# Kernel tuning notes

Hardware: AMD Instinct MI355X
Metric: run time of the kernel (lower is better)

The kernel has to match this reference:

```python
import jax, jax.numpy as jnp
import numpy as np

B, C, H, W = 4, 256, 64, 64
DQ = C // 8

def setup_inputs() -> dict:
    key = jax.random.key(0)
    ks = jax.random.split(key, 7)
    x = jax.random.normal(ks[0], (B, C, H, W), dtype=jnp.float32)
    # 1x1 convs == per-pixel linear layers: weight [out, in], bias [out]
    Wq = jax.random.normal(ks[1], (DQ, C), dtype=jnp.float32) * (1.0 / np.sqrt(C))
    bq = jax.random.normal(ks[2], (DQ,), dtype=jnp.float32) * 0.01
    Wk = jax.random.normal(ks[3], (DQ, C), dtype=jnp.float32) * (1.0 / np.sqrt(C))
    bk = jax.random.normal(ks[4], (DQ,), dtype=jnp.float32) * 0.01
    Wv = jax.random.normal(ks[5], (C, C), dtype=jnp.float32) * (1.0 / np.sqrt(C))
    bv = jax.random.normal(ks[6], (C,), dtype=jnp.float32) * 0.01
    return {"x": x, "Wq": Wq, "bq": bq, "Wk": Wk, "bk": bk, "Wv": Wv, "bv": bv}

def reference(x, Wq, bq, Wk, bk, Wv, bv):
    b, c, h, w = x.shape
    n = h * w
    xf = x.reshape(b, c, n)                                  # [b,c,n]
    Q = jnp.einsum('dc,bcn->bnd', Wq, xf) + bq               # [b,n,dq]
    K = jnp.einsum('dc,bcn->bdn', Wk, xf) + bk[None, :, None]  # [b,dq,n]
    A = jax.nn.softmax(jnp.einsum('bnd,bdm->bnm', Q, K), axis=-1)  # [b,n,n]
    V = jnp.einsum('oc,bcn->bon', Wv, xf) + bv[None, :, None]      # [b,c,n]
    # torch: bmm(V, A^T) -> out[b,c,i] = sum_j V[b,c,j] * A[b,i,j]
    out = jnp.einsum('bcj,bij->bci', V, A)
    return x + out.reshape(b, c, h, w)
```

## Files before the change

kernel.cpp:

```cpp
#include <hip/hip_runtime.h>
#include <math.h>

#define BB 4
#define CC 256
#define NN 4096
#define DQ 32
#define LOG2E 1.44269504f

typedef _Float16 half8 __attribute__((ext_vector_type(8)));
typedef _Float16 half4 __attribute__((ext_vector_type(4)));
typedef float float4v __attribute__((ext_vector_type(4)));

__global__ __launch_bounds__(64) void prep_kernel(
    const float* __restrict__ Wq, const float* __restrict__ bq,
    const float* __restrict__ Wk, const float* __restrict__ bk,
    const float* __restrict__ Wv, const float* __restrict__ bv,
    _Float16* __restrict__ Wh, float* __restrict__ bh)
{
    int o = blockIdx.x, t = threadIdx.x;
    const float* src; float scale = 1.0f, bias;
    if (o < DQ)            { src = Wq + o * CC;        scale = LOG2E; bias = bq[o] * LOG2E; }
    else if (o < 2 * DQ)   { src = Wk + (o - DQ) * CC;                bias = bk[o - DQ]; }
    else                   { src = Wv + (o - 2 * DQ) * CC;            bias = bv[o - 2 * DQ]; }
    float4 v = *(const float4*)(src + t * 4);
    half4 h = { (_Float16)(v.x * scale), (_Float16)(v.y * scale),
                (_Float16)(v.z * scale), (_Float16)(v.w * scale) };
    *(half4*)(Wh + o * CC + t * 4) = h;
    if (t == 0) bh[o] = bias;
}

__global__ __launch_bounds__(256) void proj_kernel(
    const float* __restrict__ x, const _Float16* __restrict__ Wh,
    const float* __restrict__ bh,
    _Float16* __restrict__ Qt, _Float16* __restrict__ Kt,
    _Float16* __restrict__ Vh)
{
    __shared__ _Float16 xl[32 * 256];
    __shared__ _Float16 os_qk[32 * 72];
    __shared__ _Float16 os_v[256 * 40];

    const int tid = threadIdx.x;
    const int lane = tid & 63, w = tid >> 6;
    const int i16 = lane & 15, q = lane >> 4;
    const int n0 = blockIdx.x * 32, b = blockIdx.y;

    const float* xb = x + (size_t)b * CC * NN + n0;
    #pragma unroll
    for (int u = 0; u < 8; ++u) {
        int idx = u * 256 + tid;
        int c = idx >> 3, n4 = idx & 7;
        float4 v = *(const float4*)(xb + (size_t)c * NN + n4 * 4);
        int chunk = c >> 3, cl = c & 7;
        float vv[4] = {v.x, v.y, v.z, v.w};
        #pragma unroll
        for (int e = 0; e < 4; ++e) {
            int n = n4 * 4 + e;
            xl[n * 256 + ((chunk ^ n) * 8) + cl] = (_Float16)vv[e];
        }
    }

    float4v acc[5][2];
    const int obase = 80 * w;
    #pragma unroll
    for (int ot = 0; ot < 5; ++ot) {
        float4 b4 = *(const float4*)(bh + obase + 16 * ot + 4 * q);
        #pragma unroll
        for (int nt = 0; nt < 2; ++nt)
            acc[ot][nt] = (float4v){b4.x, b4.y, b4.z, b4.w};
    }
    __syncthreads();

    #pragma unroll
    for (int k = 0; k < 8; ++k) {
        half8 af[5], bf[2];
        #pragma unroll
        for (int ot = 0; ot < 5; ++ot)
            af[ot] = *(const half8*)(Wh + (size_t)(obase + 16 * ot + i16) * CC + k * 32 + 8 * q);
        #pragma unroll
        for (int nt = 0; nt < 2; ++nt) {
            int n = 16 * nt + i16;
            bf[nt] = *(const half8*)&xl[n * 256 + (((4 * k + q) ^ n) * 8)];
        }
        #pragma unroll
        for (int ot = 0; ot < 5; ++ot)
            #pragma unroll
            for (int nt = 0; nt < 2; ++nt)
                acc[ot][nt] = __builtin_amdgcn_mfma_f32_16x16x32_f16(af[ot], bf[nt], acc[ot][nt], 0, 0, 0);
    }

    #pragma unroll
    for (int ot = 0; ot < 5; ++ot) {
        int og = obase + 16 * ot;
        #pragma unroll
        for (int nt = 0; nt < 2; ++nt) {
            int n = 16 * nt + i16;
            if (og < 64) {
                half4 hv = { (_Float16)acc[ot][nt][0], (_Float16)acc[ot][nt][1],
                             (_Float16)acc[ot][nt][2], (_Float16)acc[ot][nt][3] };
                *(half4*)&os_qk[n * 72 + og + 4 * q] = hv;
            } else {
                int cb = og - 64 + 4 * q;
                #pragma unroll
                for (int r = 0; r < 4; ++r)
                    os_v[(cb + r) * 40 + n] = (_Float16)acc[ot][nt][r];
            }
        }
    }
    __syncthreads();

    _Float16* Qtb = Qt + (size_t)b * NN * DQ;
    _Float16* Ktb = Kt + (size_t)b * NN * DQ;
    {
        int n = tid >> 3, p = tid & 7;
        half8 hv = *(const half8*)&os_qk[n * 72 + 8 * p];
        if (p < 4) *(half8*)(Qtb + (size_t)(n0 + n) * DQ + 8 * p) = hv;
        else       *(half8*)(Ktb + (size_t)(n0 + n) * DQ + 8 * (p - 4)) = hv;
    }
    _Float16* Vb = Vh + (size_t)b * CC * NN;
    #pragma unroll
    for (int u = 0; u < 4; ++u) {
        int c = u * 64 + (tid >> 2), p = tid & 3;
        half8 hv = *(const half8*)&os_v[c * 40 + 8 * p];
        *(half8*)(Vb + (size_t)c * NN + n0 + 8 * p) = hv;
    }
}

__global__ __launch_bounds__(256) void rowstat_kernel(
    const _Float16* __restrict__ Qt, const _Float16* __restrict__ Kt,
    float* __restrict__ M2, float* __restrict__ L)
{
    __shared__ _Float16 k_lds[64 * 32];
    const int tid = threadIdx.x;
    const int lane = tid & 63, w = tid >> 6;
    const int i16 = lane & 15, q = lane >> 4;
    const int q0 = blockIdx.x * 64, js = blockIdx.y, b = blockIdx.z;

    const _Float16* Qtb = Qt + (size_t)b * NN * DQ;
    const _Float16* Ktb = Kt + (size_t)b * NN * DQ;
    half8 qb = *(const half8*)(Qtb + (size_t)(q0 + 16 * w + i16) * DQ + 8 * q);

    const int jb = js * 1024;
    const int jl = tid >> 2, dg = tid & 3;
    half8 kv = *(const half8*)(Ktb + (size_t)(jb + jl) * DQ + 8 * dg);

    float m = -INFINITY, l = 0.f;
    for (int t = 0; t < 16; ++t) {
        __syncthreads();
        *(half8*)&k_lds[jl * 32 + ((dg ^ (jl & 3)) * 8)] = kv;
        __syncthreads();
        if (t < 15)
            kv = *(const half8*)(Ktb + (size_t)(jb + (t + 1) * 64 + jl) * DQ + 8 * dg);
        float4v s[4];
        __builtin_amdgcn_s_setprio(1);
        #pragma unroll
        for (int jt = 0; jt < 4; ++jt) {
            int j = 16 * jt + i16;
            half8 ka = *(const half8*)&k_lds[j * 32 + ((q ^ (j & 3)) * 8)];
            float4v z = {0.f, 0.f, 0.f, 0.f};
            s[jt] = __builtin_amdgcn_mfma_f32_16x16x32_f16(ka, qb, z, 0, 0, 0);
        }
        __builtin_amdgcn_s_setprio(0);
        float tmax = s[0][0];
        #pragma unroll
        for (int jt = 0; jt < 4; ++jt)
            #pragma unroll
            for (int r = 0; r < 4; ++r)
                tmax = fmaxf(tmax, s[jt][r]);
        float mnew = fmaxf(m, tmax);
        float sum = 0.f;
        #pragma unroll
        for (int jt = 0; jt < 4; ++jt)
            #pragma unroll
            for (int r = 0; r < 4; ++r)
                sum += exp2f(s[jt][r] - mnew);
        l = l * exp2f(m - mnew) + sum;
        m = mnew;
    }
    #pragma unroll
    for (int off = 16; off <= 32; off <<= 1) {
        float mo = __shfl_xor(m, off, 64);
        float lo = __shfl_xor(l, off, 64);
        float mn = fmaxf(m, mo);
        l = l * exp2f(m - mn) + lo * exp2f(mo - mn);
        m = mn;
    }
    if (q == 0) {
        int qi = q0 + 16 * w + i16;
        M2[((size_t)b * 4 + js) * NN + qi] = m;
        L[((size_t)b * 4 + js) * NN + qi] = l;
    }
}

__global__ __launch_bounds__(256) void attn_kernel(
    const float* __restrict__ x,
    const _Float16* __restrict__ Qt, const _Float16* __restrict__ Kt,
    const _Float16* __restrict__ Vh,
    const float* __restrict__ M2, const float* __restrict__ L,
    float* __restrict__ out)
{
    __shared__ _Float16 k_lds[64 * 32];
    __shared__ _Float16 v_lds[128 * 64];
    __shared__ _Float16 ps[32 * 72];

    const int tid = threadIdx.x;
    const int w = tid >> 6, lane = tid & 63;
    const int i16 = lane & 15, q = lane >> 4;
    const int i0 = blockIdx.x * 32, cs = blockIdx.y, b = blockIdx.z;
    const int c0 = cs * 128;

    const _Float16* Ktb = Kt + (size_t)b * NN * DQ;
    const _Float16* Vb  = Vh + (size_t)b * CC * NN + (size_t)c0 * NN;

    float m2v[2], linv[2];
    #pragma unroll
    for (int it = 0; it < 2; ++it) {
        int qi = i0 + 16 * it + i16;
        float mm = -INFINITY, ll = 0.f;
        #pragma unroll
        for (int p = 0; p < 4; ++p) {
            float mp = M2[((size_t)b * 4 + p) * NN + qi];
            float lp = L [((size_t)b * 4 + p) * NN + qi];
            float mn = fmaxf(mm, mp);
            ll = ll * exp2f(mm - mn) + lp * exp2f(mp - mn);
            mm = mn;
        }
        m2v[it] = mm;
        linv[it] = 1.0f / ll;
    }

    half8 qb[2];
    {
        const _Float16* Qtb = Qt + (size_t)b * NN * DQ;
        qb[0] = *(const half8*)(Qtb + (size_t)(i0 + i16) * DQ + 8 * q);
        qb[1] = *(const half8*)(Qtb + (size_t)(i0 + 16 + i16) * DQ + 8 * q);
    }

    float4v O[2][2];
    #pragma unroll
    for (int ct = 0; ct < 2; ++ct)
        #pragma unroll
        for (int it = 0; it < 2; ++it)
            O[ct][it] = (float4v){0.f, 0.f, 0.f, 0.f};

    const int jK = tid >> 2, dgK = tid & 3;
    const int cbV = tid >> 3, jgV = tid & 7;

    half8 kv, vv[4];
    kv = *(const half8*)(Ktb + (size_t)jK * DQ + 8 * dgK);
    #pragma unroll
    for (int u = 0; u < 4; ++u)
        vv[u] = *(const half8*)(Vb + (size_t)(u * 32 + cbV) * NN + 8 * jgV);

    for (int j0 = 0; j0 < NN; j0 += 64) {
        __syncthreads();
        *(half8*)&k_lds[jK * 32 + ((dgK ^ (jK & 3)) * 8)] = kv;
        #pragma unroll
        for (int u = 0; u < 4; ++u) {
            int c = u * 32 + cbV;
            *(half8*)&v_lds[c * 64 + ((jgV ^ (c & 7)) * 8)] = vv[u];
        }
        __syncthreads();

        if (j0 + 64 < NN) {
            kv = *(const half8*)(Ktb + (size_t)(j0 + 64 + jK) * DQ + 8 * dgK);
            #pragma unroll
            for (int u = 0; u < 4; ++u)
                vv[u] = *(const half8*)(Vb + (size_t)(u * 32 + cbV) * NN + (j0 + 64) + 8 * jgV);
        }

        {
            int j = 16 * w + i16;
            half8 ka = *(const half8*)&k_lds[j * 32 + ((q ^ (j & 3)) * 8)];
            #pragma unroll
            for (int it = 0; it < 2; ++it) {
                float4v z = {0.f, 0.f, 0.f, 0.f};
                float4v s = __builtin_amdgcn_mfma_f32_16x16x32_f16(ka, qb[it], z, 0, 0, 0);
                half4 hv = { (_Float16)exp2f(s[0] - m2v[it]),
                             (_Float16)exp2f(s[1] - m2v[it]),
                             (_Float16)exp2f(s[2] - m2v[it]),
                             (_Float16)exp2f(s[3] - m2v[it]) };
                *(half4*)&ps[(16 * it + i16) * 72 + 16 * w + 4 * q] = hv;
            }
        }
        __syncthreads();

        half8 pb[2][2];
        #pragma unroll
        for (int ks = 0; ks < 2; ++ks)
            #pragma unroll
            for (int it = 0; it < 2; ++it)
                pb[ks][it] = *(const half8*)&ps[(16 * it + i16) * 72 + 32 * ks + 8 * q];
        __builtin_amdgcn_s_setprio(1);
        #pragma unroll
        for (int ct = 0; ct < 2; ++ct) {
            int c = 32 * w + 16 * ct + i16;
            #pragma unroll
            for (int ks = 0; ks < 2; ++ks) {
                int g = 4 * ks + q;
                half8 va = *(const half8*)&v_lds[c * 64 + ((g ^ (c & 7)) * 8)];
                #pragma unroll
                for (int it = 0; it < 2; ++it)
                    O[ct][it] = __builtin_amdgcn_mfma_f32_16x16x32_f16(va, pb[ks][it], O[ct][it], 0, 0, 0);
            }
        }
        __builtin_amdgcn_s_setprio(0);
    }

    const float* xb = x + (size_t)b * CC * NN;
    float* ob = out + (size_t)b * CC * NN;
    #pragma unroll
    for (int ct = 0; ct < 2; ++ct)
        #pragma unroll
        for (int it = 0; it < 2; ++it)
            #pragma unroll
            for (int r = 0; r < 4; ++r) {
                int c = c0 + 32 * w + 16 * ct + 4 * q + r;
                size_t idx = (size_t)c * NN + i0 + 16 * it + i16;
                ob[idx] = xb[idx] + O[ct][it][r] * linv[it];
            }
}

extern "C" void kernel_launch(void* const* d_in, const int* in_sizes, int n_in,
                              void* d_out, int out_size, void* d_ws, size_t ws_size,
                              hipStream_t stream) {
    const float* x  = (const float*)d_in[0];
    const float* Wq = (const float*)d_in[1];
    const float* bq = (const float*)d_in[2];
    const float* Wk = (const float*)d_in[3];
    const float* bk = (const float*)d_in[4];
    const float* Wv = (const float*)d_in[5];
    const float* bv = (const float*)d_in[6];
    float* out = (float*)d_out;

    char* ws = (char*)d_ws;
    _Float16* Wh = (_Float16*)(ws);
    float*    bh = (float*)(ws + 163840);
    _Float16* Qt = (_Float16*)(ws + 262144);
    _Float16* Kt = (_Float16*)(ws + 1310720);
    _Float16* Vh = (_Float16*)(ws + 2359296);
    float*    M2 = (float*)(ws + 10747904);
    float*    L  = (float*)(ws + 11010048);

    prep_kernel<<<dim3(320), 64, 0, stream>>>(Wq, bq, Wk, bk, Wv, bv, Wh, bh);
    proj_kernel<<<dim3(NN / 32, BB), 256, 0, stream>>>(x, Wh, bh, Qt, Kt, Vh);
    rowstat_kernel<<<dim3(NN / 64, 4, BB), 256, 0, stream>>>(Qt, Kt, M2, L);
    attn_kernel<<<dim3(NN / 32, 2, BB), 256, 0, stream>>>(x, Qt, Kt, Vh, M2, L, out);
}
```

Measured before the change: 202.5 us.

## Fuse softmax row statistics into attention via online softmax with double-buffered LDS

Removes the separate rowstat pass that recomputed Q·K over all keys to get the row max and sum. The attention kernel now keeps a running max and sum per row, combining per-wave partial stats through a small shared buffer each tile, and rescales the accumulators and P fragments. K/V tiles are double-buffered in LDS so the next tile's global loads overlap compute, with a single barrier pair per iteration. This adds per-tile shuffles, exp2 rescales and extra LDS traffic, and uses more LDS per block, which may lower occupancy.

```diff
diff --git a/kernel.cpp b/kernel.cpp
--- a/kernel.cpp
+++ b/kernel.cpp
@@ -10,6 +10,7 @@
 typedef _Float16 half8 __attribute__((ext_vector_type(8)));
 typedef _Float16 half4 __attribute__((ext_vector_type(4)));
 typedef float float4v __attribute__((ext_vector_type(4)));
+typedef float float2v __attribute__((ext_vector_type(2)));
 
 __global__ __launch_bounds__(64) void prep_kernel(
     const float* __restrict__ Wq, const float* __restrict__ bq,
@@ -125,82 +126,16 @@
     }
 }
 
-__global__ __launch_bounds__(256) void rowstat_kernel(
-    const _Float16* __restrict__ Qt, const _Float16* __restrict__ Kt,
-    float* __restrict__ M2, float* __restrict__ L)
-{
-    __shared__ _Float16 k_lds[64 * 32];
-    const int tid = threadIdx.x;
-    const int lane = tid & 63, w = tid >> 6;
-    const int i16 = lane & 15, q = lane >> 4;
-    const int q0 = blockIdx.x * 64, js = blockIdx.y, b = blockIdx.z;
-
-    const _Float16* Qtb = Qt + (size_t)b * NN * DQ;
-    const _Float16* Ktb = Kt + (size_t)b * NN * DQ;
-    half8 qb = *(const half8*)(Qtb + (size_t)(q0 + 16 * w + i16) * DQ + 8 * q);
-
-    const int jb = js * 1024;
-    const int jl = tid >> 2, dg = tid & 3;
-    half8 kv = *(const half8*)(Ktb + (size_t)(jb + jl) * DQ + 8 * dg);
-
-    float m = -INFINITY, l = 0.f;
-    for (int t = 0; t < 16; ++t) {
-        __syncthreads();
-        *(half8*)&k_lds[jl * 32 + ((dg ^ (jl & 3)) * 8)] = kv;
-        __syncthreads();
-        if (t < 15)
-            kv = *(const half8*)(Ktb + (size_t)(jb + (t + 1) * 64 + jl) * DQ + 8 * dg);
-        float4v s[4];
-        __builtin_amdgcn_s_setprio(1);
-        #pragma unroll
-        for (int jt = 0; jt < 4; ++jt) {
-            int j = 16 * jt + i16;
-            half8 ka = *(const half8*)&k_lds[j * 32 + ((q ^ (j & 3)) * 8)];
-            float4v z = {0.f, 0.f, 0.f, 0.f};
-            s[jt] = __builtin_amdgcn_mfma_f32_16x16x32_f16(ka, qb, z, 0, 0, 0);
-        }
-        __builtin_amdgcn_s_setprio(0);
-        float tmax = s[0][0];
-        #pragma unroll
-        for (int jt = 0; jt < 4; ++jt)
-            #pragma unroll
-            for (int r = 0; r < 4; ++r)
-                tmax = fmaxf(tmax, s[jt][r]);
-        float mnew = fmaxf(m, tmax);
-        float sum = 0.f;
-        #pragma unroll
-        for (int jt = 0; jt < 4; ++jt)
-            #pragma unroll
-            for (int r = 0; r < 4; ++r)
-                sum += exp2f(s[jt][r] - mnew);
-        l = l * exp2f(m - mnew) + sum;
-        m = mnew;
-    }
-    #pragma unroll
-    for (int off = 16; off <= 32; off <<= 1) {
-        float mo = __shfl_xor(m, off, 64);
-        float lo = __shfl_xor(l, off, 64);
-        float mn = fmaxf(m, mo);
-        l = l * exp2f(m - mn) + lo * exp2f(mo - mn);
-        m = mn;
-    }
-    if (q == 0) {
-        int qi = q0 + 16 * w + i16;
-        M2[((size_t)b * 4 + js) * NN + qi] = m;
-        L[((size_t)b * 4 + js) * NN + qi] = l;
-    }
-}
-
 __global__ __launch_bounds__(256) void attn_kernel(
     const float* __restrict__ x,
     const _Float16* __restrict__ Qt, const _Float16* __restrict__ Kt,
     const _Float16* __restrict__ Vh,
-    const float* __restrict__ M2, const float* __restrict__ L,
     float* __restrict__ out)
 {
-    __shared__ _Float16 k_lds[64 * 32];
-    __shared__ _Float16 v_lds[128 * 64];
+    __shared__ _Float16 k_lds[2][64 * 32];
+    __shared__ _Float16 v_lds[2][128 * 64];
     __shared__ _Float16 ps[32 * 72];
+    __shared__ float    st[32][10];
 
     const int tid = threadIdx.x;
     const int w = tid >> 6, lane = tid & 63;
@@ -211,23 +146,6 @@
     const _Float16* Ktb = Kt + (size_t)b * NN * DQ;
     const _Float16* Vb  = Vh + (size_t)b * CC * NN + (size_t)c0 * NN;
 
-    float m2v[2], linv[2];
-    #pragma unroll
-    for (int it = 0; it < 2; ++it) {
-        int qi = i0 + 16 * it + i16;
-        float mm = -INFINITY, ll = 0.f;
-        #pragma unroll
-        for (int p = 0; p < 4; ++p) {
-            float mp = M2[((size_t)b * 4 + p) * NN + qi];
-            float lp = L [((size_t)b * 4 + p) * NN + qi];
-            float mn = fmaxf(mm, mp);
-            ll = ll * exp2f(mm - mn) + lp * exp2f(mp - mn);
-            mm = mn;
-        }
-        m2v[it] = mm;
-        linv[it] = 1.0f / ll;
-    }
-
     half8 qb[2];
     {
         const _Float16* Qtb = Qt + (size_t)b * NN * DQ;
@@ -241,46 +159,72 @@
         #pragma unroll
         for (int it = 0; it < 2; ++it)
             O[ct][it] = (float4v){0.f, 0.f, 0.f, 0.f};
+    float m_run[2] = {-INFINITY, -INFINITY};
+    float l_run[2] = {0.f, 0.f};
 
     const int jK = tid >> 2, dgK = tid & 3;
     const int cbV = tid >> 3, jgV = tid & 7;
+    const int kaddr = jK * 32 + ((dgK ^ (jK & 3)) * 8);
+    int vaddr[4];
+    #pragma unroll
+    for (int u = 0; u < 4; ++u) {
+        int c = u * 32 + cbV;
+        vaddr[u] = c * 64 + ((jgV ^ (c & 7)) * 8);
+    }
 
     half8 kv, vv[4];
     kv = *(const half8*)(Ktb + (size_t)jK * DQ + 8 * dgK);
     #pragma unroll
     for (int u = 0; u < 4; ++u)
         vv[u] = *(const half8*)(Vb + (size_t)(u * 32 + cbV) * NN + 8 * jgV);
-
-    for (int j0 = 0; j0 < NN; j0 += 64) {
-        __syncthreads();
-        *(half8*)&k_lds[jK * 32 + ((dgK ^ (jK & 3)) * 8)] = kv;
-        #pragma unroll
-        for (int u = 0; u < 4; ++u) {
-            int c = u * 32 + cbV;
-            *(half8*)&v_lds[c * 64 + ((jgV ^ (c & 7)) * 8)] = vv[u];
-        }
-        __syncthreads();
-
-        if (j0 + 64 < NN) {
-            kv = *(const half8*)(Ktb + (size_t)(j0 + 64 + jK) * DQ + 8 * dgK);
+    *(half8*)&k_lds[0][kaddr] = kv;
+    #pragma unroll
+    for (int u = 0; u < 4; ++u)
+        *(half8*)&v_lds[0][vaddr[u]] = vv[u];
+    kv = *(const half8*)(Ktb + (size_t)(64 + jK) * DQ + 8 * dgK);
+    #pragma unroll
+    for (int u = 0; u < 4; ++u)
+        vv[u] = *(const half8*)(Vb + (size_t)(u * 32 + cbV) * NN + 64 + 8 * jgV);
+    __syncthreads();
+
+    for (int t = 0; t < 64; ++t) {
+        const int cur = t & 1;
+
+        if (t < 63) {
+            *(half8*)&k_lds[cur ^ 1][kaddr] = kv;
             #pragma unroll
             for (int u = 0; u < 4; ++u)
-                vv[u] = *(const half8*)(Vb + (size_t)(u * 32 + cbV) * NN + (j0 + 64) + 8 * jgV);
-        }
-
+                *(half8*)&v_lds[cur ^ 1][vaddr[u]] = vv[u];
+        }
         {
             int j = 16 * w + i16;
-            half8 ka = *(const half8*)&k_lds[j * 32 + ((q ^ (j & 3)) * 8)];
+            half8 ka = *(const half8*)&k_lds[cur][j * 32 + ((q ^ (j & 3)) * 8)];
             #pragma unroll
             for (int it = 0; it < 2; ++it) {
                 float4v z = {0.f, 0.f, 0.f, 0.f};
                 float4v s = __builtin_amdgcn_mfma_f32_16x16x32_f16(ka, qb[it], z, 0, 0, 0);
-                half4 hv = { (_Float16)exp2f(s[0] - m2v[it]),
-                             (_Float16)exp2f(s[1] - m2v[it]),
-                             (_Float16)exp2f(s[2] - m2v[it]),
-                             (_Float16)exp2f(s[3] - m2v[it]) };
+                float mx = fmaxf(fmaxf(s[0], s[1]), fmaxf(s[2], s[3]));
+                mx = fmaxf(mx, __shfl_xor(mx, 16));
+                mx = fmaxf(mx, __shfl_xor(mx, 32));
+                float p0 = exp2f(s[0] - mx), p1 = exp2f(s[1] - mx);
+                float p2 = exp2f(s[2] - mx), p3 = exp2f(s[3] - mx);
+                float sm = (p0 + p1) + (p2 + p3);
+                sm += __shfl_xor(sm, 16);
+                sm += __shfl_xor(sm, 32);
+                half4 hv = { (_Float16)p0, (_Float16)p1, (_Float16)p2, (_Float16)p3 };
                 *(half4*)&ps[(16 * it + i16) * 72 + 16 * w + 4 * q] = hv;
+                if (q == 0) {
+                    st[16 * it + i16][2 * w]     = mx;
+                    st[16 * it + i16][2 * w + 1] = sm;
+                }
             }
+        }
+        if (t < 62) {
+            int jn = (t + 2) * 64;
+            kv = *(const half8*)(Ktb + (size_t)(jn + jK) * DQ + 8 * dgK);
+            #pragma unroll
+            for (int u = 0; u < 4; ++u)
+                vv[u] = *(const half8*)(Vb + (size_t)(u * 32 + cbV) * NN + jn + 8 * jgV);
         }
         __syncthreads();
 
@@ -290,6 +234,31 @@
             #pragma unroll
             for (int it = 0; it < 2; ++it)
                 pb[ks][it] = *(const half8*)&ps[(16 * it + i16) * 72 + 32 * ks + 8 * q];
+
+        #pragma unroll
+        for (int it = 0; it < 2; ++it) {
+            const float* sr = &st[16 * it + i16][0];
+            float2v a0 = *(const float2v*)&sr[0];
+            float2v a1 = *(const float2v*)&sr[2];
+            float2v a2 = *(const float2v*)&sr[4];
+            float2v a3 = *(const float2v*)&sr[6];
+            float mt = fmaxf(fmaxf(a0[0], a1[0]), fmaxf(a2[0], a3[0]));
+            float mn = fmaxf(m_run[it], mt);
+            float al = exp2f(m_run[it] - mn);
+            float lt = a0[1] * exp2f(a0[0] - mn) + a1[1] * exp2f(a1[0] - mn)
+                     + a2[1] * exp2f(a2[0] - mn) + a3[1] * exp2f(a3[0] - mn);
+            l_run[it] = l_run[it] * al + lt;
+            m_run[it] = mn;
+            O[0][it] *= al;
+            O[1][it] *= al;
+            float msA = (q & 2) ? a1[0] : a0[0];
+            float msB = (q & 2) ? a3[0] : a2[0];
+            _Float16 bA = (_Float16)exp2f(msA - mn);
+            _Float16 bB = (_Float16)exp2f(msB - mn);
+            pb[0][it] *= bA;
+            pb[1][it] *= bB;
+        }
+
         __builtin_amdgcn_s_setprio(1);
         #pragma unroll
         for (int ct = 0; ct < 2; ++ct) {
@@ -297,15 +266,17 @@
             #pragma unroll
             for (int ks = 0; ks < 2; ++ks) {
                 int g = 4 * ks + q;
-                half8 va = *(const half8*)&v_lds[c * 64 + ((g ^ (c & 7)) * 8)];
+                half8 va = *(const half8*)&v_lds[cur][c * 64 + ((g ^ (c & 7)) * 8)];
                 #pragma unroll
                 for (int it = 0; it < 2; ++it)
                     O[ct][it] = __builtin_amdgcn_mfma_f32_16x16x32_f16(va, pb[ks][it], O[ct][it], 0, 0, 0);
             }
         }
         __builtin_amdgcn_s_setprio(0);
-    }
-
+        __syncthreads();
+    }
+
+    float linv[2] = { 1.0f / l_run[0], 1.0f / l_run[1] };
     const float* xb = x + (size_t)b * CC * NN;
     float* ob = out + (size_t)b * CC * NN;
     #pragma unroll
@@ -338,11 +309,8 @@
     _Float16* Qt = (_Float16*)(ws + 262144);
     _Float16* Kt = (_Float16*)(ws + 1310720);
     _Float16* Vh = (_Float16*)(ws + 2359296);
-    float*    M2 = (float*)(ws + 10747904);
-    float*    L  = (float*)(ws + 11010048);
 
     prep_kernel<<<dim3(320), 64, 0, stream>>>(Wq, bq, Wk, bk, Wv, bv, Wh, bh);
     proj_kernel<<<dim3(NN / 32, BB), 256, 0, stream>>>(x, Wh, bh, Qt, Kt, Vh);
-    rowstat_kernel<<<dim3(NN / 64, 4, BB), 256, 0, stream>>>(Qt, Kt, M2, L);
-    attn_kernel<<<dim3(NN / 32, 2, BB), 256, 0, stream>>>(x, Qt, Kt, Vh, M2, L, out);
+    attn_kernel<<<dim3(NN / 32, 2, BB), 256, 0, stream>>>(x, Qt, Kt, Vh, out);
 }
```

After: 285.4 us. 40.9% more time.

## Pipeline attention QK/PV stages with multi-buffered LDS and drop softmax max rescaling

Applied to the files above, without the earlier changes.

The attention kernel now processes 64 query rows per block and software-pipelines the loop: K and V tiles are double- and triple-buffered in LDS, and P tiles are double-buffered, so the PV MFMA of the previous tile overlaps the QK/exp of the current one with one barrier per iteration. The rowstat kernel drops LDS and online rescaling, reading K fragments straight from global with register prefetch and summing raw exp2 values. The final max is folded into the normalizer. This removes barriers and exp work, but summing unshifted exp2 risks overflow for large logits and the larger tile uses more LDS and registers, which lowers occupancy.

```diff
diff --git a/kernel.cpp b/kernel.cpp
--- a/kernel.cpp
+++ b/kernel.cpp
@@ -129,61 +129,37 @@
     const _Float16* __restrict__ Qt, const _Float16* __restrict__ Kt,
     float* __restrict__ M2, float* __restrict__ L)
 {
-    __shared__ _Float16 k_lds[64 * 32];
     const int tid = threadIdx.x;
     const int lane = tid & 63, w = tid >> 6;
     const int i16 = lane & 15, q = lane >> 4;
     const int q0 = blockIdx.x * 64, js = blockIdx.y, b = blockIdx.z;
 
     const _Float16* Qtb = Qt + (size_t)b * NN * DQ;
-    const _Float16* Ktb = Kt + (size_t)b * NN * DQ;
+    const _Float16* kb  = Kt + (size_t)b * NN * DQ + (size_t)(js * 1024) * DQ;
     half8 qb = *(const half8*)(Qtb + (size_t)(q0 + 16 * w + i16) * DQ + 8 * q);
 
-    const int jb = js * 1024;
-    const int jl = tid >> 2, dg = tid & 3;
-    half8 kv = *(const half8*)(Ktb + (size_t)(jb + jl) * DQ + 8 * dg);
+    half8 ka[4];
+    #pragma unroll
+    for (int u = 0; u < 4; ++u)
+        ka[u] = *(const half8*)(kb + (size_t)(16 * u + i16) * DQ + 8 * q);
 
     float m = -INFINITY, l = 0.f;
-    for (int t = 0; t < 16; ++t) {
-        __syncthreads();
-        *(half8*)&k_lds[jl * 32 + ((dg ^ (jl & 3)) * 8)] = kv;
-        __syncthreads();
-        if (t < 15)
-            kv = *(const half8*)(Ktb + (size_t)(jb + (t + 1) * 64 + jl) * DQ + 8 * dg);
-        float4v s[4];
-        __builtin_amdgcn_s_setprio(1);
-        #pragma unroll
-        for (int jt = 0; jt < 4; ++jt) {
-            int j = 16 * jt + i16;
-            half8 ka = *(const half8*)&k_lds[j * 32 + ((q ^ (j & 3)) * 8)];
+    for (int t = 0; t < 64; t += 4) {
+        #pragma unroll
+        for (int u = 0; u < 4; ++u) {
             float4v z = {0.f, 0.f, 0.f, 0.f};
-            s[jt] = __builtin_amdgcn_mfma_f32_16x16x32_f16(ka, qb, z, 0, 0, 0);
-        }
-        __builtin_amdgcn_s_setprio(0);
-        float tmax = s[0][0];
-        #pragma unroll
-        for (int jt = 0; jt < 4; ++jt)
-            #pragma unroll
-            for (int r = 0; r < 4; ++r)
-                tmax = fmaxf(tmax, s[jt][r]);
-        float mnew = fmaxf(m, tmax);
-        float sum = 0.f;
-        #pragma unroll
-        for (int jt = 0; jt < 4; ++jt)
-            #pragma unroll
-            for (int r = 0; r < 4; ++r)
-                sum += exp2f(s[jt][r] - mnew);
-        l = l * exp2f(m - mnew) + sum;
-        m = mnew;
-    }
-    #pragma unroll
-    for (int off = 16; off <= 32; off <<= 1) {
-        float mo = __shfl_xor(m, off, 64);
-        float lo = __shfl_xor(l, off, 64);
-        float mn = fmaxf(m, mo);
-        l = l * exp2f(m - mn) + lo * exp2f(mo - mn);
-        m = mn;
-    }
+            float4v s = __builtin_amdgcn_mfma_f32_16x16x32_f16(ka[u], qb, z, 0, 0, 0);
+            int nt = t + 4 + u;
+            if (nt < 64)
+                ka[u] = *(const half8*)(kb + (size_t)(16 * nt + i16) * DQ + 8 * q);
+            m = fmaxf(m, fmaxf(fmaxf(s[0], s[1]), fmaxf(s[2], s[3])));
+            l += (exp2f(s[0]) + exp2f(s[1])) + (exp2f(s[2]) + exp2f(s[3]));
+        }
+    }
+    l += __shfl_xor(l, 16, 64);
+    l += __shfl_xor(l, 32, 64);
+    m = fmaxf(m, __shfl_xor(m, 16, 64));
+    m = fmaxf(m, __shfl_xor(m, 32, 64));
     if (q == 0) {
         int qi = q0 + 16 * w + i16;
         M2[((size_t)b * 4 + js) * NN + qi] = m;
@@ -198,112 +174,127 @@
     const float* __restrict__ M2, const float* __restrict__ L,
     float* __restrict__ out)
 {
-    __shared__ _Float16 k_lds[64 * 32];
-    __shared__ _Float16 v_lds[128 * 64];
-    __shared__ _Float16 ps[32 * 72];
+    __shared__ _Float16 k_lds[2][64 * 32];
+    __shared__ _Float16 v_lds[3][128 * 64];
+    __shared__ _Float16 ps[2][64 * 72];
 
     const int tid = threadIdx.x;
     const int w = tid >> 6, lane = tid & 63;
     const int i16 = lane & 15, q = lane >> 4;
-    const int i0 = blockIdx.x * 32, cs = blockIdx.y, b = blockIdx.z;
+    const int i0 = blockIdx.x * 64, cs = blockIdx.y, b = blockIdx.z;
     const int c0 = cs * 128;
 
     const _Float16* Ktb = Kt + (size_t)b * NN * DQ;
     const _Float16* Vb  = Vh + (size_t)b * CC * NN + (size_t)c0 * NN;
 
-    float m2v[2], linv[2];
-    #pragma unroll
-    for (int it = 0; it < 2; ++it) {
+    float m2v[4], linv[4];
+    #pragma unroll
+    for (int it = 0; it < 4; ++it) {
         int qi = i0 + 16 * it + i16;
         float mm = -INFINITY, ll = 0.f;
         #pragma unroll
         for (int p = 0; p < 4; ++p) {
-            float mp = M2[((size_t)b * 4 + p) * NN + qi];
-            float lp = L [((size_t)b * 4 + p) * NN + qi];
-            float mn = fmaxf(mm, mp);
-            ll = ll * exp2f(mm - mn) + lp * exp2f(mp - mn);
-            mm = mn;
+            mm = fmaxf(mm, M2[((size_t)b * 4 + p) * NN + qi]);
+            ll += L[((size_t)b * 4 + p) * NN + qi];
         }
         m2v[it] = mm;
-        linv[it] = 1.0f / ll;
-    }
-
-    half8 qb[2];
+        linv[it] = exp2f(mm) / ll;
+    }
+
+    half8 qb[4];
     {
         const _Float16* Qtb = Qt + (size_t)b * NN * DQ;
-        qb[0] = *(const half8*)(Qtb + (size_t)(i0 + i16) * DQ + 8 * q);
-        qb[1] = *(const half8*)(Qtb + (size_t)(i0 + 16 + i16) * DQ + 8 * q);
-    }
-
-    float4v O[2][2];
+        #pragma unroll
+        for (int it = 0; it < 4; ++it)
+            qb[it] = *(const half8*)(Qtb + (size_t)(i0 + 16 * it + i16) * DQ + 8 * q);
+    }
+
+    float4v O[2][4];
     #pragma unroll
     for (int ct = 0; ct < 2; ++ct)
         #pragma unroll
-        for (int it = 0; it < 2; ++it)
+        for (int it = 0; it < 4; ++it)
             O[ct][it] = (float4v){0.f, 0.f, 0.f, 0.f};
 
     const int jK = tid >> 2, dgK = tid & 3;
     const int cbV = tid >> 3, jgV = tid & 7;
+    const int kaddr = jK * 32 + ((dgK ^ (jK & 3)) * 8);
+    int vaddr[4];
+    #pragma unroll
+    for (int u = 0; u < 4; ++u) {
+        int c = u * 32 + cbV;
+        vaddr[u] = c * 64 + ((jgV ^ (c & 7)) * 8);
+    }
 
     half8 kv, vv[4];
     kv = *(const half8*)(Ktb + (size_t)jK * DQ + 8 * dgK);
     #pragma unroll
     for (int u = 0; u < 4; ++u)
         vv[u] = *(const half8*)(Vb + (size_t)(u * 32 + cbV) * NN + 8 * jgV);
-
-    for (int j0 = 0; j0 < NN; j0 += 64) {
+    *(half8*)&k_lds[0][kaddr] = kv;
+    #pragma unroll
+    for (int u = 0; u < 4; ++u)
+        *(half8*)&v_lds[0][vaddr[u]] = vv[u];
+    kv = *(const half8*)(Ktb + (size_t)(64 + jK) * DQ + 8 * dgK);
+    #pragma unroll
+    for (int u = 0; u < 4; ++u)
+        vv[u] = *(const half8*)(Vb + (size_t)(u * 32 + cbV) * NN + 64 + 8 * jgV);
+
+    for (int t = 0; t <= 64; ++t) {
         __syncthreads();
-        *(half8*)&k_lds[jK * 32 + ((dgK ^ (jK & 3)) * 8)] = kv;
-        #pragma unroll
-        for (int u = 0; u < 4; ++u) {
-            int c = u * 32 + cbV;
-            *(half8*)&v_lds[c * 64 + ((jgV ^ (c & 7)) * 8)] = vv[u];
-        }
-        __syncthreads();
-
-        if (j0 + 64 < NN) {
-            kv = *(const half8*)(Ktb + (size_t)(j0 + 64 + jK) * DQ + 8 * dgK);
+        if (t < 63) {
+            *(half8*)&k_lds[(t + 1) & 1][kaddr] = kv;
+            const int vn = (t + 1) % 3;
             #pragma unroll
             for (int u = 0; u < 4; ++u)
-                vv[u] = *(const half8*)(Vb + (size_t)(u * 32 + cbV) * NN + (j0 + 64) + 8 * jgV);
-        }
-
-        {
+                *(half8*)&v_lds[vn][vaddr[u]] = vv[u];
+        }
+        if (t < 62) {
+            int jn = (t + 2) * 64;
+            kv = *(const half8*)(Ktb + (size_t)(jn + jK) * DQ + 8 * dgK);
+            #pragma unroll
+            for (int u = 0; u < 4; ++u)
+                vv[u] = *(const half8*)(Vb + (size_t)(u * 32 + cbV) * NN + jn + 8 * jgV);
+        }
+        if (t > 0) {
+            const _Float16* psp = ps[(t - 1) & 1];
+            const _Float16* vp  = v_lds[(t - 1) % 3];
+            half8 pb[2][4];
+            #pragma unroll
+            for (int ks = 0; ks < 2; ++ks)
+                #pragma unroll
+                for (int it = 0; it < 4; ++it)
+                    pb[ks][it] = *(const half8*)&psp[(16 * it + i16) * 72 + 32 * ks + 8 * q];
+            __builtin_amdgcn_s_setprio(1);
+            #pragma unroll
+            for (int ct = 0; ct < 2; ++ct) {
+                int c = 32 * w + 16 * ct + i16;
+                #pragma unroll
+                for (int ks = 0; ks < 2; ++ks) {
+                    int g = 4 * ks + q;
+                    half8 va = *(const half8*)&vp[c * 64 + ((g ^ (c & 7)) * 8)];
+                    #pragma unroll
+                    for (int it = 0; it < 4; ++it)
+                        O[ct][it] = __builtin_amdgcn_mfma_f32_16x16x32_f16(va, pb[ks][it], O[ct][it], 0, 0, 0);
+                }
+            }
+            __builtin_amdgcn_s_setprio(0);
+        }
+        if (t < 64) {
             int j = 16 * w + i16;
-            half8 ka = *(const half8*)&k_lds[j * 32 + ((q ^ (j & 3)) * 8)];
-            #pragma unroll
-            for (int it = 0; it < 2; ++it) {
+            half8 ka = *(const half8*)&k_lds[t & 1][j * 32 + ((q ^ (j & 3)) * 8)];
+            _Float16* psc = ps[t & 1];
+            #pragma unroll
+            for (int it = 0; it < 4; ++it) {
                 float4v z = {0.f, 0.f, 0.f, 0.f};
                 float4v s = __builtin_amdgcn_mfma_f32_16x16x32_f16(ka, qb[it], z, 0, 0, 0);
                 half4 hv = { (_Float16)exp2f(s[0] - m2v[it]),
                              (_Float16)exp2f(s[1] - m2v[it]),
                              (_Float16)exp2f(s[2] - m2v[it]),
                              (_Float16)exp2f(s[3] - m2v[it]) };
-                *(half4*)&ps[(16 * it + i16) * 72 + 16 * w + 4 * q] = hv;
+                *(half4*)&psc[(16 * it + i16) * 72 + 16 * w + 4 * q] = hv;
             }
         }
-        __syncthreads();
-
-        half8 pb[2][2];
-        #pragma unroll
-        for (int ks = 0; ks < 2; ++ks)
-            #pragma unroll
-            for (int it = 0; it < 2; ++it)
-                pb[ks][it] = *(const half8*)&ps[(16 * it + i16) * 72 + 32 * ks + 8 * q];
-        __builtin_amdgcn_s_setprio(1);
-        #pragma unroll
-        for (int ct = 0; ct < 2; ++ct) {
-            int c = 32 * w + 16 * ct + i16;
-            #pragma unroll
-            for (int ks = 0; ks < 2; ++ks) {
-                int g = 4 * ks + q;
-                half8 va = *(const half8*)&v_lds[c * 64 + ((g ^ (c & 7)) * 8)];
-                #pragma unroll
-                for (int it = 0; it < 2; ++it)
-                    O[ct][it] = __builtin_amdgcn_mfma_f32_16x16x32_f16(va, pb[ks][it], O[ct][it], 0, 0, 0);
-            }
-        }
-        __builtin_amdgcn_s_setprio(0);
     }
 
     const float* xb = x + (size_t)b * CC * NN;
@@ -311,7 +302,7 @@
     #pragma unroll
     for (int ct = 0; ct < 2; ++ct)
         #pragma unroll
-        for (int it = 0; it < 2; ++it)
+        for (int it = 0; it < 4; ++it)
             #pragma unroll
             for (int r = 0; r < 4; ++r) {
                 int c = c0 + 32 * w + 16 * ct + 4 * q + r;
@@ -344,5 +335,5 @@
     prep_kernel<<<dim3(320), 64, 0, stream>>>(Wq, bq, Wk, bk, Wv, bv, Wh, bh);
     proj_kernel<<<dim3(NN / 32, BB), 256, 0, stream>>>(x, Wh, bh, Qt, Kt, Vh);
     rowstat_kernel<<<dim3(NN / 64, 4, BB), 256, 0, stream>>>(Qt, Kt, M2, L);
-    attn_kernel<<<dim3(NN / 32, 2, BB), 256, 0, stream>>>(x, Qt, Kt, Vh, M2, L, out);
-}
+    attn_kernel<<<dim3(NN / 64, 2, BB), 256, 0, stream>>>(x, Qt, Kt, Vh, M2, L, out);
+}
```

Result: faster. 196.3 us (-3.1%).
